# Optimization experiments

Hardware: AMD Instinct MI355X
Metric: run time of the kernel (lower is better)

The kernel has to match this reference:

```python
import jax, jax.numpy as jnp
import numpy as np

B, S, D, H, SE, DE, DFF = 4, 1024, 1024, 16, 77, 768, 4096


def _ln(x, g, b, eps=1e-5):
    mu = jnp.mean(x, axis=-1, keepdims=True)
    var = jnp.mean((x - mu) ** 2, axis=-1, keepdims=True)
    return (x - mu) * jax.lax.rsqrt(var + eps) * g + b


def _split_heads(x, heads):
    b, s, d = x.shape
    return x.reshape(b, s, heads, d // heads).transpose(0, 2, 1, 3)  # b h s hd


def _attn(q, k, v, heads):
    # memory_efficient_attention equivalent: softmax(q k^T * scale) v, per head
    q, k, v = _split_heads(q, heads), _split_heads(k, heads), _split_heads(v, heads)
    scale = q.shape[-1] ** -0.5
    scores = jnp.einsum('bhqd,bhkd->bhqk', q, k) * scale
    probs = jax.nn.softmax(scores, axis=-1)
    o = jnp.einsum('bhqk,bhkd->bhqd', probs, v)
    b, h, s, hd = o.shape
    return o.transpose(0, 2, 1, 3).reshape(b, s, h * hd)


def _geglu_ff(x, w1, b1, w2, b2):
    proj = x @ w1 + b1
    a, gate = jnp.split(proj, 2, axis=-1)
    return (a * jax.nn.gelu(gate)) @ w2 + b2


def _forward(h1, h2, enc, wq, wk, wv, wqc, wo, bo, ln1g, ln1b, ln2g, ln2b,
             w2q, w2k, w2v, w2o, b2o, wff1, bff1, wff2, bff2):
    # norm1
    n1 = _ln(h1, ln1g[0], ln1b[0])
    n2 = _ln(h2, ln1g[1], ln1b[1])
    # dual-stream uni-direction attention (self + cross with swapped K/V)
    q1, k1, v1, q1c = n1 @ wq[0], n1 @ wk[0], n1 @ wv[0], n1 @ wqc[0]
    q2, k2, v2, q2c = n2 @ wq[1], n2 @ wk[1], n2 @ wv[1], n2 @ wqc[1]
    a1 = _attn(q1, k1, v1, H) + _attn(q1c, k2, v2, H)
    a2 = _attn(q2, k2, v2, H) + _attn(q2c, k1, v1, H)
    a1 = a1 @ wo[0] + bo[0]
    a2 = a2 @ wo[1] + bo[1]
    h1 = h1 + a1
    h2 = h2 + a2
    # cross attention to encoder states (attn2)
    n1 = _ln(h1, ln2g[0], ln2b[0])
    n2 = _ln(h2, ln2g[1], ln2b[1])
    c1 = _attn(n1 @ w2q[0], enc @ w2k[0], enc @ w2v[0], H) @ w2o[0] + b2o[0]
    c2 = _attn(n2 @ w2q[1], enc @ w2k[1], enc @ w2v[1], H) @ w2o[1] + b2o[1]
    h1 = h1 + c1
    h2 = h2 + c2
    # feed-forward (GEGLU), applied to norm2 output exactly as in source
    h1 = h1 + _geglu_ff(n1, wff1[0], bff1[0], wff2[0], bff2[0])
    h2 = h2 + _geglu_ff(n2, wff1[1], bff1[1], wff2[1], bff2[1])
    return (h1, h2)


def setup_inputs() -> dict:
    key = jax.random.key(0)
    ks = jax.random.split(key, 16)
    f = lambda k, shp: jax.random.normal(k, shp, jnp.float32) * 0.02
    return {
        'h1': jax.random.normal(ks[0], (B, S, D), jnp.float32),
        'h2': jax.random.normal(ks[1], (B, S, D), jnp.float32),
        'enc': jax.random.normal(ks[2], (B, SE, DE), jnp.float32),
        'wq': f(ks[3], (2, D, D)), 'wk': f(ks[4], (2, D, D)),
        'wv': f(ks[5], (2, D, D)), 'wqc': f(ks[6], (2, D, D)),
        'wo': f(ks[7], (2, D, D)), 'bo': jnp.zeros((2, D), jnp.float32),
        'ln1g': jnp.ones((2, D), jnp.float32), 'ln1b': jnp.zeros((2, D), jnp.float32),
        'ln2g': jnp.ones((2, D), jnp.float32), 'ln2b': jnp.zeros((2, D), jnp.float32),
        'w2q': f(ks[8], (2, D, D)), 'w2k': f(ks[9], (2, DE, D)),
        'w2v': f(ks[10], (2, DE, D)), 'w2o': f(ks[11], (2, D, D)),
        'b2o': jnp.zeros((2, D), jnp.float32),
        'wff1': f(ks[12], (2, D, 2 * DFF)), 'bff1': jnp.zeros((2, 2 * DFF), jnp.float32),
        'wff2': f(ks[13], (2, DFF, D)), 'bff2': jnp.zeros((2, D), jnp.float32),
    }


def reference(h1, h2, enc, wq, wk, wv, wqc, wo, bo, ln1g, ln1b, ln2g, ln2b,
              w2q, w2k, w2v, w2o, b2o, wff1, bff1, wff2, bff2):
    return _forward(h1, h2, enc, wq, wk, wv, wqc, wo, bo, ln1g, ln1b, ln2g, ln2b,
                    w2q, w2k, w2v, w2o, b2o, wff1, bff1, wff2, bff2)
```

## Files before the change

kernel.cpp:

```cpp
#include <hip/hip_runtime.h>

typedef unsigned short u16;
typedef short v8s __attribute__((ext_vector_type(8)));
typedef float v4f __attribute__((ext_vector_type(4)));

__device__ __forceinline__ float bf2f(u16 u) {
  union { unsigned u; float f; } c; c.u = ((unsigned)u) << 16; return c.f;
}
__device__ __forceinline__ u16 f2bf(float x) {
  union { float f; unsigned u; } c; c.f = x;
  unsigned r = c.u + 0x7fffu + ((c.u >> 16) & 1u);
  return (u16)(r >> 16);
}
__device__ __forceinline__ v4f vzero() { v4f z; z[0]=0.f; z[1]=0.f; z[2]=0.f; z[3]=0.f; return z; }
__device__ __forceinline__ v4f mfma16(v8s a, v8s b, v4f c) {
  return __builtin_amdgcn_mfma_f32_16x16x32_bf16(a, b, c, 0, 0, 0);
}
__device__ __forceinline__ void async_lds16(const void* g, void* l) {
  __builtin_amdgcn_global_load_lds((__attribute__((address_space(1))) void*)g,
                                   (__attribute__((address_space(3))) void*)l, 16, 0, 0);
}
__device__ __forceinline__ float gelu_f(float x) {
  return 0.5f * x * (1.f + tanhf(0.7978845608028654f * (x + 0.044715f * x * x * x)));
}

__global__ void detect_k(const unsigned* __restrict__ p, unsigned* __restrict__ flag) {
  if (threadIdx.x == 0) {
    flag[0] = (p[0] == 0x3F803F80u) ? 1u : 0u;
    flag[1] = 0u;
  }
}

__global__ __launch_bounds__(256) void cvt_k(const unsigned* __restrict__ flag,
    const void* __restrict__ src, u16* __restrict__ dst, int n) {
  int i = (blockIdx.x * 256 + threadIdx.x) * 8;
  if (i >= n) return;
  if (*flag) {
    *(uint4*)(dst + i) = *(const uint4*)((const u16*)src + i);
  } else {
    const float* s = (const float*)src + i;
    #pragma unroll
    for (int j = 0; j < 8; ++j) dst[i + j] = f2bf(s[j]);
  }
}

__global__ __launch_bounds__(256) void tr_k(const unsigned* __restrict__ flag,
    const void* __restrict__ in, u16* __restrict__ out, int R, int C, long outZS) {
  __shared__ u16 tile[32][33];
  size_t zin = (size_t)blockIdx.z * R * C;
  size_t zout = (size_t)blockIdx.z * outZS;
  int c0 = blockIdx.x * 32, r0 = blockIdx.y * 32;
  int tx = threadIdx.x & 31, ty = threadIdx.x >> 5;
  unsigned isbf = *flag;
  const u16* inb = (const u16*)in + zin;
  const float* inf = (const float*)in + zin;
  #pragma unroll
  for (int i = ty; i < 32; i += 8) {
    size_t idx = (size_t)(r0 + i) * C + c0 + tx;
    tile[i][tx] = isbf ? inb[idx] : f2bf(inf[idx]);
  }
  __syncthreads();
  out += zout;
  #pragma unroll
  for (int i = ty; i < 32; i += 8) out[(size_t)(c0 + i) * R + r0 + tx] = tile[tx][i];
}

__global__ __launch_bounds__(256) void vtr_k(const u16* __restrict__ in, u16* __restrict__ out) {
  __shared__ u16 tile[32][33];
  int z = blockIdx.z >> 2, b = blockIdx.z & 3;
  const u16* ip = in + (size_t)z * 16777216 + (size_t)b * 4194304 + 2048;
  u16* op = out + (size_t)z * 4194304 + (size_t)b * 1048576;
  int k0 = blockIdx.x * 32, d0 = blockIdx.y * 32;
  int tx = threadIdx.x & 31, ty = threadIdx.x >> 5;
  #pragma unroll
  for (int i = ty; i < 32; i += 8)
    tile[i][tx] = ip[(size_t)(k0 + i) * 4096 + d0 + tx];
  __syncthreads();
  #pragma unroll
  for (int i = ty; i < 32; i += 8)
    op[(size_t)(d0 + i) * 1024 + k0 + tx] = tile[tx][i];
}

__global__ __launch_bounds__(256) void ln_k(const unsigned* __restrict__ flag,
    const void* __restrict__ src0, const void* __restrict__ src1,
    const u16* __restrict__ gw, const u16* __restrict__ bw, u16* __restrict__ out) {
  int z = blockIdx.y;
  const void* src = z ? src1 : src0;
  out += (size_t)z * 4194304; gw += z * 1024; bw += z * 1024;
  int row = blockIdx.x, t = threadIdx.x;
  unsigned isbf = *flag;
  float4 v;
  if (isbf) {
    uint2 d = ((const uint2*)((const u16*)src + (size_t)row * 1024))[t];
    v.x = bf2f((u16)(d.x & 0xffffu)); v.y = bf2f((u16)(d.x >> 16));
    v.z = bf2f((u16)(d.y & 0xffffu)); v.w = bf2f((u16)(d.y >> 16));
  } else {
    v = ((const float4*)((const float*)src + (size_t)row * 1024))[t];
  }
  float s = v.x + v.y + v.z + v.w;
  float s2 = v.x * v.x + v.y * v.y + v.z * v.z + v.w * v.w;
  #pragma unroll
  for (int o = 32; o; o >>= 1) { s += __shfl_down(s, o); s2 += __shfl_down(s2, o); }
  __shared__ float red[8];
  int w = t >> 6;
  if ((t & 63) == 0) { red[w] = s; red[4 + w] = s2; }
  __syncthreads();
  if (t == 0) {
    red[0] = red[0] + red[1] + red[2] + red[3];
    red[4] = red[4] + red[5] + red[6] + red[7];
  }
  __syncthreads();
  float mu = red[0] * (1.f / 1024.f);
  float var = red[4] * (1.f / 1024.f) - mu * mu;
  float rstd = rsqrtf(var + 1e-5f);
  int c = t * 4;
  float xs[4] = { v.x, v.y, v.z, v.w };
  #pragma unroll
  for (int j = 0; j < 4; ++j) {
    float g = bf2f(gw[c + j]), bb = bf2f(bw[c + j]);
    out[(size_t)row * 1024 + c + j] = f2bf((xs[j] - mu) * rstd * g + bb);
  }
}

template<int EPI>
__global__ __launch_bounds__(256, 2) void gemm_bt(
    const u16* __restrict__ A, const u16* __restrict__ Bt,
    int M, int N, int K, int lda, int ldb, int ldc,
    const u16* __restrict__ bias, const u16* aux,
    float* __restrict__ resF, void* __restrict__ outB,
    long zsA, long zsB, long zsC, int zsBias,
    const void* rin0, const void* rin1,
    const unsigned* __restrict__ flagp)
{
  int z = blockIdx.z;
  A += (size_t)z * zsA;
  Bt += (size_t)z * zsB;
  size_t zc = (size_t)z * zsC;
  unsigned isbf = 0;
  if (EPI == 4 || EPI == 5) isbf = *flagp;
  const void* rin = (EPI == 5) ? (z ? rin1 : rin0) : nullptr;
  __shared__ alignas(16) u16 As[128 * 64];
  __shared__ alignas(16) u16 Bs[128 * 64];
  int tid = threadIdx.x;
  int lane = tid & 63, wave = tid >> 6;
  int l15 = lane & 15, l4 = lane >> 4;
  int wm = wave & 1, wn = wave >> 1;
  int m0 = blockIdx.x * 128, n0 = blockIdx.y * 128;
  v4f acc[4][4];
  #pragma unroll
  for (int i = 0; i < 4; ++i)
    #pragma unroll
    for (int j = 0; j < 4; ++j) acc[i][j] = vzero();

  for (int k0 = 0; k0 < K; k0 += 64) {
    #pragma unroll
    for (int it = 0; it < 4; ++it) {
      int sidx = it * 256 + tid;
      int r = sidx >> 3, cs = (sidx & 7) * 8;
      int ra = m0 + r; if (ra > M - 1) ra = M - 1;
      async_lds16(A + (size_t)ra * lda + k0 + cs, As + (size_t)(it * 256 + wave * 64) * 8);
      async_lds16(Bt + (size_t)(n0 + r) * ldb + k0 + cs, Bs + (size_t)(it * 256 + wave * 64) * 8);
    }
    __syncthreads();
    #pragma unroll
    for (int ks = 0; ks < 2; ++ks) {
      v8s af[4], bfr[4];
      #pragma unroll
      for (int i = 0; i < 4; ++i) {
        af[i]  = *(const v8s*)(As + (wm * 64 + i * 16 + l15) * 64 + ks * 32 + l4 * 8);
        bfr[i] = *(const v8s*)(Bs + (wn * 64 + i * 16 + l15) * 64 + ks * 32 + l4 * 8);
      }
      #pragma unroll
      for (int i = 0; i < 4; ++i)
        #pragma unroll
        for (int j = 0; j < 4; ++j)
          acc[i][j] = mfma16(af[i], bfr[j], acc[i][j]);
    }
    __syncthreads();
  }
  #pragma unroll
  for (int mt = 0; mt < 4; ++mt) {
    #pragma unroll
    for (int r = 0; r < 4; ++r) {
      int gr = m0 + wm * 64 + mt * 16 + l4 * 4 + r;
      if (gr >= M) continue;
      size_t ri = (size_t)gr * ldc;
      size_t ro = zc + ri;
      #pragma unroll
      for (int nt = 0; nt < 4; ++nt) {
        int gc = n0 + wn * 64 + nt * 16 + l15;
        float v = acc[mt][nt][r];
        if (bias) v += bf2f(bias[(size_t)z * zsBias + gc]);
        if (EPI == 0) ((u16*)outB)[ro + gc] = f2bf(v);
        else if (EPI == 1) ((u16*)outB)[ro + gc] = f2bf(gelu_f(v));
        else if (EPI == 2) ((u16*)outB)[ro + gc] = f2bf(v * bf2f(aux[ro + gc]));
        else if (EPI == 3) resF[ro + gc] += v;
        else if (EPI == 5) {
          float h = isbf ? bf2f(((const u16*)rin)[ri + gc]) : ((const float*)rin)[ri + gc];
          resF[ro + gc] = h + v;
        } else {
          float o = resF[ro + gc] + v;
          if (isbf) ((u16*)outB)[ro + gc] = f2bf(o);
          else ((float*)outB)[ro + gc] = o;
        }
      }
    }
  }
}

__global__ __launch_bounds__(256, 2) void flash_self_k(
    const u16* __restrict__ qkv, const u16* __restrict__ Vt, u16* __restrict__ O)
{
  __shared__ alignas(16) u16 Ksh[128 * 64];
  __shared__ alignas(16) u16 Vsh[64 * 128];
  __shared__ alignas(16) u16 Psh[4][16 * 128];
  int tid = threadIdx.x, lane = tid & 63, wave = tid >> 6;
  int l15 = lane & 15, l4 = lane >> 4;
  int h = blockIdx.y;
  int strm = blockIdx.z >> 2, b = blockIdx.z & 3;
  const size_t ZS = 16777216;
  const size_t BS = 4194304;
  int q0 = blockIdx.x * 64 + wave * 16;
  u16* pw = Psh[wave];
  int swz = l15 & 7;
  v4f res[4];
  #pragma unroll
  for (int i = 0; i < 4; ++i) res[i] = vzero();

  for (int sg = 0; sg < 2; ++sg) {
    int qcol = sg ? 3072 : 0;
    int ksrc = sg ? (strm ^ 1) : strm;
    const u16* Qb = qkv + (size_t)strm * ZS + (size_t)b * BS + qcol + h * 64;
    const u16* Kb = qkv + (size_t)ksrc * ZS + (size_t)b * BS + 1024 + h * 64;
    const u16* Vb = Vt + (size_t)ksrc * BS + (size_t)b * 1048576 + h * 65536;
    v8s qf0 = *(const v8s*)(Qb + (size_t)(q0 + l15) * 4096 + l4 * 8);
    v8s qf1 = *(const v8s*)(Qb + (size_t)(q0 + l15) * 4096 + l4 * 8 + 32);
    v4f oacc[4];
    #pragma unroll
    for (int i = 0; i < 4; ++i) oacc[i] = vzero();
    float mrun[4], lrun[4];
    #pragma unroll
    for (int r = 0; r < 4; ++r) { mrun[r] = -1e30f; lrun[r] = 0.f; }

    for (int c0 = 0; c0 < 1024; c0 += 128) {
      #pragma unroll
      for (int it = 0; it < 4; ++it) {
        int sidx = it * 256 + tid;
        int r = sidx >> 3, c = sidx & 7;
        async_lds16(Kb + (size_t)(c0 + r) * 4096 + ((c ^ (r & 7)) * 8),
                    Ksh + (size_t)(it * 256 + wave * 64) * 8);
      }
      #pragma unroll
      for (int it = 0; it < 4; ++it) {
        int sidx = it * 256 + tid;
        int d = sidx >> 4, c = sidx & 15;
        async_lds16(Vb + (size_t)d * 1024 + c0 + ((c ^ (d & 15)) * 8),
                    Vsh + (size_t)(it * 256 + wave * 64) * 8);
      }
      __syncthreads();
      v4f s[4][2];
      #pragma unroll
      for (int g = 0; g < 4; ++g) { s[g][0] = vzero(); s[g][1] = vzero(); }
      __builtin_amdgcn_s_setprio(1);
      #pragma unroll
      for (int g = 0; g < 4; ++g) {
        int rb0 = (g * 32 + l15) * 64, rb1 = rb0 + 16 * 64;
        v8s k00 = *(const v8s*)(Ksh + rb0 + ((l4 ^ swz) * 8));
        v8s k10 = *(const v8s*)(Ksh + rb1 + ((l4 ^ swz) * 8));
        v8s k01 = *(const v8s*)(Ksh + rb0 + (((4 + l4) ^ swz) * 8));
        v8s k11 = *(const v8s*)(Ksh + rb1 + (((4 + l4) ^ swz) * 8));
        s[g][0] = mfma16(qf0, k00, s[g][0]);
        s[g][1] = mfma16(qf0, k10, s[g][1]);
        s[g][0] = mfma16(qf1, k01, s[g][0]);
        s[g][1] = mfma16(qf1, k11, s[g][1]);
      }
      __builtin_amdgcn_s_setprio(0);
      float alpha[4];
      #pragma unroll
      for (int r = 0; r < 4; ++r) {
        int row = l4 * 4 + r;
        float x[8];
        #pragma unroll
        for (int g = 0; g < 4; ++g) {
          x[2 * g]     = s[g][0][r] * 0.125f;
          x[2 * g + 1] = s[g][1][r] * 0.125f;
        }
        float tm = fmaxf(fmaxf(fmaxf(x[0], x[1]), fmaxf(x[2], x[3])),
                         fmaxf(fmaxf(x[4], x[5]), fmaxf(x[6], x[7])));
        #pragma unroll
        for (int o = 8; o; o >>= 1) tm = fmaxf(tm, __shfl_xor(tm, o));
        float mn = fmaxf(mrun[r], tm);
        alpha[r] = __expf(mrun[r] - mn);
        mrun[r] = mn;
        float rs = 0.f;
        #pragma unroll
        for (int j = 0; j < 8; ++j) {
          float p = __expf(x[j] - mn);
          rs += p;
          int col = (j >> 1) * 32 + (j & 1) * 16 + l15;
          pw[row * 128 + (((col >> 3) ^ row) * 8) + (col & 7)] = f2bf(p);
        }
        #pragma unroll
        for (int o = 8; o; o >>= 1) rs += __shfl_xor(rs, o);
        lrun[r] = lrun[r] * alpha[r] + rs;
      }
      #pragma unroll
      for (int nt = 0; nt < 4; ++nt)
        #pragma unroll
        for (int r = 0; r < 4; ++r) oacc[nt][r] *= alpha[r];
      __builtin_amdgcn_s_setprio(1);
      #pragma unroll
      for (int g = 0; g < 4; ++g) {
        v8s pa = *(const v8s*)(pw + l15 * 128 + (((g * 4 + l4) ^ l15) * 8));
        #pragma unroll
        for (int nt = 0; nt < 4; ++nt) {
          int vr = nt * 16 + l15;
          v8s vb = *(const v8s*)(Vsh + vr * 128 + (((g * 4 + l4) ^ (vr & 15)) * 8));
          oacc[nt] = mfma16(pa, vb, oacc[nt]);
        }
      }
      __builtin_amdgcn_s_setprio(0);
      __syncthreads();
    }
    #pragma unroll
    for (int r = 0; r < 4; ++r) {
      float inv = 1.f / lrun[r];
      #pragma unroll
      for (int nt = 0; nt < 4; ++nt) res[nt][r] += oacc[nt][r] * inv;
    }
  }
  #pragma unroll
  for (int nt = 0; nt < 4; ++nt) {
    #pragma unroll
    for (int r = 0; r < 4; ++r) {
      int gq = q0 + l4 * 4 + r;
      size_t oi = (size_t)strm * BS + ((size_t)b * 1024 + gq) * 1024 + h * 64 + nt * 16 + l15;
      O[oi] = f2bf(res[nt][r]);
    }
  }
}

__global__ __launch_bounds__(256, 2) void flash_cross_k(
    const u16* __restrict__ Q, const u16* __restrict__ KV, u16* __restrict__ O)
{
  __shared__ alignas(16) u16 Ksh[128 * 64];
  __shared__ alignas(16) unsigned VshT[64 * 68];
  __shared__ alignas(16) u16 Psh[4][16 * 128];
  int tid = threadIdx.x, lane = tid & 63, wave = tid >> 6;
  int l15 = lane & 15, l4 = lane >> 4;
  int h = blockIdx.y;
  int strm = blockIdx.z >> 2, b = blockIdx.z & 3;
  const u16* Qb = Q + (size_t)strm * 4194304 + (size_t)b * 1048576 + h * 64;
  const u16* Kb = KV + (size_t)strm * 630784 + (size_t)b * 157696 + h * 64;
  const u16* Vb = Kb + 1024;
  int q0 = blockIdx.x * 64 + wave * 16;
  u16* pw = Psh[wave];
  int swz = l15 & 7;
  v8s qf0 = *(const v8s*)(Qb + (size_t)(q0 + l15) * 1024 + l4 * 8);
  v8s qf1 = *(const v8s*)(Qb + (size_t)(q0 + l15) * 1024 + l4 * 8 + 32);

  #pragma unroll
  for (int it = 0; it < 4; ++it) {
    int sidx = it * 256 + tid;
    int r = sidx >> 3, c = sidx & 7;
    int gk = r > 76 ? 76 : r;
    async_lds16(Kb + (size_t)gk * 2048 + ((c ^ (r & 7)) * 8),
                Ksh + (size_t)(it * 256 + wave * 64) * 8);
  }
  #pragma unroll
  for (int it = 0; it < 2; ++it) {
    int tt = it * 256 + tid;
    int kp = tt & 63, dsg = tt >> 6;
    int gk0 = kp * 2, gk1 = kp * 2 + 1;
    if (gk0 > 76) gk0 = 76;
    if (gk1 > 76) gk1 = 76;
    v8s v0 = *(const v8s*)(Vb + (size_t)gk0 * 2048 + dsg * 8);
    v8s v1 = *(const v8s*)(Vb + (size_t)gk1 * 2048 + dsg * 8);
    #pragma unroll
    for (int j = 0; j < 8; ++j) {
      unsigned pk = (unsigned)(u16)v0[j] | ((unsigned)(u16)v1[j] << 16);
      VshT[(dsg * 8 + j) * 68 + kp] = pk;
    }
  }
  __syncthreads();
  v4f s[4][2];
  #pragma unroll
  for (int g = 0; g < 4; ++g) { s[g][0] = vzero(); s[g][1] = vzero(); }
  __builtin_amdgcn_s_setprio(1);
  #pragma unroll
  for (int g = 0; g < 4; ++g) {
    int rb0 = (g * 32 + l15) * 64, rb1 = rb0 + 16 * 64;
    v8s k00 = *(const v8s*)(Ksh + rb0 + ((l4 ^ swz) * 8));
    v8s k10 = *(const v8s*)(Ksh + rb1 + ((l4 ^ swz) * 8));
    v8s k01 = *(const v8s*)(Ksh + rb0 + (((4 + l4) ^ swz) * 8));
    v8s k11 = *(const v8s*)(Ksh + rb1 + (((4 + l4) ^ swz) * 8));
    s[g][0] = mfma16(qf0, k00, s[g][0]);
    s[g][1] = mfma16(qf0, k10, s[g][1]);
    s[g][0] = mfma16(qf1, k01, s[g][0]);
    s[g][1] = mfma16(qf1, k11, s[g][1]);
  }
  __builtin_amdgcn_s_setprio(0);
  float lsum[4];
  #pragma unroll
  for (int r = 0; r < 4; ++r) {
    int row = l4 * 4 + r;
    float x[8];
    #pragma unroll
    for (int g = 0; g < 4; ++g) {
      bool ok0 = (g * 32 + l15) < 77, ok1 = (g * 32 + 16 + l15) < 77;
      x[2 * g]     = ok0 ? s[g][0][r] * 0.125f : -1e30f;
      x[2 * g + 1] = ok1 ? s[g][1][r] * 0.125f : -1e30f;
    }
    float tm = fmaxf(fmaxf(fmaxf(x[0], x[1]), fmaxf(x[2], x[3])),
                     fmaxf(fmaxf(x[4], x[5]), fmaxf(x[6], x[7])));
    #pragma unroll
    for (int o = 8; o; o >>= 1) tm = fmaxf(tm, __shfl_xor(tm, o));
    float rs = 0.f;
    #pragma unroll
    for (int j = 0; j < 8; ++j) {
      float p = __expf(x[j] - tm);
      rs += p;
      int col = (j >> 1) * 32 + (j & 1) * 16 + l15;
      pw[row * 128 + (((col >> 3) ^ row) * 8) + (col & 7)] = f2bf(p);
    }
    #pragma unroll
    for (int o = 8; o; o >>= 1) rs += __shfl_xor(rs, o);
    lsum[r] = rs;
  }
  v4f oacc[4];
  #pragma unroll
  for (int i = 0; i < 4; ++i) oacc[i] = vzero();
  __builtin_amdgcn_s_setprio(1);
  #pragma unroll
  for (int g = 0; g < 4; ++g) {
    v8s pa = *(const v8s*)(pw + l15 * 128 + (((g * 4 + l4) ^ l15) * 8));
    #pragma unroll
    for (int nt = 0; nt < 4; ++nt) {
      v8s vb = *(const v8s*)((const u16*)VshT + (nt * 16 + l15) * 136 + g * 32 + l4 * 8);
      oacc[nt] = mfma16(pa, vb, oacc[nt]);
    }
  }
  __builtin_amdgcn_s_setprio(0);
  #pragma unroll
  for (int nt = 0; nt < 4; ++nt) {
    #pragma unroll
    for (int r = 0; r < 4; ++r) {
      int gq = q0 + l4 * 4 + r;
      size_t oi = (size_t)strm * 4194304 + ((size_t)b * 1024 + gq) * 1024 + h * 64 + nt * 16 + l15;
      O[oi] = f2bf(oacc[nt][r] / lsum[r]);
    }
  }
}

extern "C" void kernel_launch(void* const* d_in, const int* in_sizes, int n_in,
                              void* d_out, int out_size, void* d_ws, size_t ws_size,
                              hipStream_t stream)
{
  (void)in_sizes; (void)n_in; (void)out_size;
  const void* h1   = d_in[0];
  const void* h2   = d_in[1];
  const void* enc  = d_in[2];
  const void* wq   = d_in[3];
  const void* wk   = d_in[4];
  const void* wv   = d_in[5];
  const void* wqc  = d_in[6];
  const void* wo   = d_in[7];
  const void* bo   = d_in[8];
  const void* ln1g = d_in[9];
  const void* ln1b = d_in[10];
  const void* ln2g = d_in[11];
  const void* ln2b = d_in[12];
  const void* w2q  = d_in[13];
  const void* w2k  = d_in[14];
  const void* w2v  = d_in[15];
  const void* w2o  = d_in[16];
  const void* b2o  = d_in[17];
  const void* wff1 = d_in[18];
  const void* bff1 = d_in[19];
  const void* wff2 = d_in[20];
  const void* bff2 = d_in[21];

  const size_t S1 = 4194304;
  const size_t W1 = 1048576;
  const size_t QS = 16777216;
  const size_t NE = 236544;

  char* base = (char*)d_ws;
  size_t off = 0;
  auto AL = [&](size_t n) { size_t r = off; off += (n + 255) & ~(size_t)255; return r; };
  size_t o_flag   = AL(256);
  size_t o_pb     = AL(30720 * 2);
  size_t o_encB   = AL(NE * 2);
  size_t o_wqkvT  = AL(2 * 4 * W1 * 2);
  size_t o_woT    = AL(2 * W1 * 2);
  size_t o_w2qT   = AL(2 * W1 * 2);
  size_t o_w2oT   = AL(2 * W1 * 2);
  size_t o_w2kvT  = AL(2 * 2048 * 768 * 2);
  size_t o_wff1T  = AL(2 * 8192 * 1024 * 2);
  size_t o_wff2T  = AL(2 * 4096 * 1024 * 2);
  size_t o_hw     = AL(2 * S1 * 4);
  size_t o_n      = AL(2 * S1 * 2);
  size_t o_qkv    = AL(2 * QS * 2);
  size_t o_ab     = AL(2 * S1 * 2);
  if (ws_size < off) return;

  unsigned* flagp = (unsigned*)(base + o_flag);
  const unsigned* zerop = flagp + 1;
  u16* pb = (u16*)(base + o_pb);
  u16* boB   = pb + 0;
  u16* b2oB  = pb + 2048;
  u16* ln1gB = pb + 4096;
  u16* ln1bB = pb + 6144;
  u16* ln2gB = pb + 8192;
  u16* ln2bB = pb + 10240;
  u16* bff2B = pb + 12288;
  u16* bff1B = pb + 14336;
  u16* encB  = (u16*)(base + o_encB);
  u16* wqkvT = (u16*)(base + o_wqkvT);
  u16* woT   = (u16*)(base + o_woT);
  u16* w2qT  = (u16*)(base + o_w2qT);
  u16* w2oT  = (u16*)(base + o_w2oT);
  u16* w2kvT = (u16*)(base + o_w2kvT);
  u16* wff1T = (u16*)(base + o_wff1T);
  u16* wff2T = (u16*)(base + o_wff2T);
  float* hw  = (float*)(base + o_hw);
  u16* n1    = (u16*)(base + o_n);
  u16* qkv   = (u16*)(base + o_qkv);
  u16* a1b   = (u16*)(base + o_ab);
  u16* q1x   = qkv;
  u16* c1b   = qkv + 2 * S1;
  u16* kencv = qkv + 4 * S1;
  u16* gelu  = qkv;
  u16* vtb   = n1;

  auto tr = [&](const void* ip, u16* op, int R, int C, long outZS) {
    dim3 g(C / 32, R / 32, 2);
    tr_k<<<g, 256, 0, stream>>>(flagp, ip, op, R, C, outZS);
  };
  auto cvt = [&](const void* ip, u16* op, int n) {
    cvt_k<<<(n / 8 + 255) / 256, 256, 0, stream>>>(flagp, ip, op, n);
  };
  auto gemm = [&](int epi, const u16* Ap, const u16* Bp, int M, int N, int K,
                  int lda, int ldb, int ldc, const u16* bias, const u16* aux,
                  float* resF, void* oB, int nz, long zsA, long zsB, long zsC, int zsBias,
                  const void* rin0, const void* rin1) {
    dim3 g((M + 127) / 128, N / 128, nz);
    switch (epi) {
      case 0: gemm_bt<0><<<g, 256, 0, stream>>>(Ap, Bp, M, N, K, lda, ldb, ldc, bias, aux, resF, oB, zsA, zsB, zsC, zsBias, rin0, rin1, flagp); break;
      case 1: gemm_bt<1><<<g, 256, 0, stream>>>(Ap, Bp, M, N, K, lda, ldb, ldc, bias, aux, resF, oB, zsA, zsB, zsC, zsBias, rin0, rin1, flagp); break;
      case 2: gemm_bt<2><<<g, 256, 0, stream>>>(Ap, Bp, M, N, K, lda, ldb, ldc, bias, aux, resF, oB, zsA, zsB, zsC, zsBias, rin0, rin1, flagp); break;
      case 3: gemm_bt<3><<<g, 256, 0, stream>>>(Ap, Bp, M, N, K, lda, ldb, ldc, bias, aux, resF, oB, zsA, zsB, zsC, zsBias, rin0, rin1, flagp); break;
      case 4: gemm_bt<4><<<g, 256, 0, stream>>>(Ap, Bp, M, N, K, lda, ldb, ldc, bias, aux, resF, oB, zsA, zsB, zsC, zsBias, rin0, rin1, flagp); break;
      default: gemm_bt<5><<<g, 256, 0, stream>>>(Ap, Bp, M, N, K, lda, ldb, ldc, bias, aux, resF, oB, zsA, zsB, zsC, zsBias, rin0, rin1, flagp); break;
    }
  };

  detect_k<<<1, 64, 0, stream>>>((const unsigned*)ln1g, flagp);
  cvt(bo, boB, 2048);     cvt(b2o, b2oB, 2048);
  cvt(ln1g, ln1gB, 2048); cvt(ln1b, ln1bB, 2048);
  cvt(ln2g, ln2gB, 2048); cvt(ln2b, ln2bB, 2048);
  cvt(bff2, bff2B, 2048); cvt(bff1, bff1B, 16384);
  cvt(enc, encB, (int)NE);
  tr(wq,  wqkvT + 0 * W1, 1024, 1024, 4 * (long)W1);
  tr(wk,  wqkvT + 1 * W1, 1024, 1024, 4 * (long)W1);
  tr(wv,  wqkvT + 2 * W1, 1024, 1024, 4 * (long)W1);
  tr(wqc, wqkvT + 3 * W1, 1024, 1024, 4 * (long)W1);
  tr(wo,  woT,  1024, 1024, (long)W1);
  tr(w2q, w2qT, 1024, 1024, (long)W1);
  tr(w2o, w2oT, 1024, 1024, (long)W1);
  tr(w2k, w2kvT + 0,          768, 1024, 2048L * 768);
  tr(w2v, w2kvT + 1024 * 768, 768, 1024, 2048L * 768);
  tr(wff1, wff1T, 1024, 8192, 8192L * 1024);
  tr(wff2, wff2T, 4096, 1024, 4096L * 1024);
  ln_k<<<dim3(4096, 2), 256, 0, stream>>>(flagp, h1, h2, ln1gB, ln1bB, n1);
  gemm(0, n1, wqkvT, 4096, 4096, 1024, 1024, 1024, 4096, nullptr, nullptr, nullptr, qkv,
       2, (long)S1, 4 * (long)W1, (long)QS, 0, nullptr, nullptr);
  vtr_k<<<dim3(32, 32, 8), 256, 0, stream>>>(qkv, vtb);
  flash_self_k<<<dim3(16, 16, 8), 256, 0, stream>>>(qkv, vtb, a1b);
  gemm(5, a1b, woT, 4096, 1024, 1024, 1024, 1024, 1024, boB, nullptr, hw, nullptr,
       2, (long)S1, (long)W1, (long)S1, 1024, h1, h2);
  ln_k<<<dim3(4096, 2), 256, 0, stream>>>(zerop, hw, hw + S1, ln2gB, ln2bB, n1);
  gemm(0, n1, w2qT, 4096, 1024, 1024, 1024, 1024, 1024, nullptr, nullptr, nullptr, q1x,
       2, (long)S1, (long)W1, (long)S1, 0, nullptr, nullptr);
  gemm(0, encB, w2kvT, 308, 2048, 768, 768, 768, 2048, nullptr, nullptr, nullptr, kencv,
       2, 0, 2048L * 768, 308L * 2048, 0, nullptr, nullptr);
  flash_cross_k<<<dim3(16, 16, 8), 256, 0, stream>>>(q1x, kencv, c1b);
  gemm(3, c1b, w2oT, 4096, 1024, 1024, 1024, 1024, 1024, b2oB, nullptr, hw, nullptr,
       2, (long)S1, (long)W1, (long)S1, 1024, nullptr, nullptr);
  gemm(1, n1, wff1T + 4096 * 1024, 4096, 4096, 1024, 1024, 1024, 4096,
       bff1B + 4096, nullptr, nullptr, gelu, 2, (long)S1, 8192L * 1024, (long)QS, 8192,
       nullptr, nullptr);
  gemm(2, n1, wff1T, 4096, 4096, 1024, 1024, 1024, 4096,
       bff1B, gelu, nullptr, gelu, 2, (long)S1, 8192L * 1024, (long)QS, 8192,
       nullptr, nullptr);
  gemm(4, gelu, wff2T, 4096, 1024, 4096, 4096, 4096, 1024,
       bff2B, nullptr, hw, d_out, 2, (long)QS, 4096L * 1024, (long)S1, 1024,
       nullptr, nullptr);
}
```

Baseline: 1.222 ms.

## Add 256x256-tile 8-wave GEMM with 4-stage async pipeline for large projections

Introduces a new GEMM kernel with 256x256 output tiles, 512 threads, and a 4-slot LDS ring filled by async global-to-LDS loads using explicit vmcnt gating and priority hints. It is used for the QKV projection and the two GEGLU first-layer GEMMs, which are all N=4096, K=1024. The larger tile raises arithmetic intensity and cuts redundant operand loads. The cost is 128 KB of LDS per block, heavy accumulator register pressure, and only 512 blocks per launch, which may reduce occupancy or leave some tail imbalance.

```diff
diff --git a/kernel.cpp b/kernel.cpp
--- a/kernel.cpp
+++ b/kernel.cpp
@@ -203,6 +203,151 @@
           if (isbf) ((u16*)outB)[ro + gc] = f2bf(o);
           else ((float*)outB)[ro + gc] = o;
         }
+      }
+    }
+  }
+}
+
+template<int EPI>
+__global__ __launch_bounds__(512, 2) void gemm256(
+    const u16* __restrict__ A, const u16* __restrict__ Bt,
+    int M, int N, int K, int lda, int ldb, int ldc,
+    const u16* __restrict__ bias, const u16* aux, void* __restrict__ outB,
+    long zsA, long zsB, long zsC, int zsBias)
+{
+  __shared__ alignas(16) u16 As[4][8192];
+  __shared__ alignas(16) u16 Bs[4][8192];
+  int z = blockIdx.z;
+  A += (size_t)z * zsA;
+  Bt += (size_t)z * zsB;
+  size_t zc = (size_t)z * zsC;
+  int tid = threadIdx.x, lane = tid & 63, wave = tid >> 6;
+  int l15 = lane & 15, l4 = lane >> 4;
+  int wm = wave >> 2, wn = wave & 3;
+  int m0 = blockIdx.x * 256, n0 = blockIdx.y * 256;
+  int sa = l4 ^ ((l15 >> 1) & 3);
+  int nG = K >> 5;
+
+  v4f acc[8][4];
+  #pragma unroll
+  for (int i = 0; i < 8; ++i)
+    #pragma unroll
+    for (int j = 0; j < 4; ++j) acc[i][j] = vzero();
+
+  auto stageA = [&](int g) {
+    int sl = g & 3;
+    #pragma unroll
+    for (int l = 0; l < 2; ++l) {
+      int sidx = l * 512 + tid;
+      int r = sidx >> 2, c = sidx & 3;
+      async_lds16(A + (size_t)(m0 + r) * lda + g * 32 + ((c ^ ((sidx >> 3) & 3)) * 8),
+                  As[sl] + (size_t)(l * 512 + wave * 64) * 8);
+    }
+  };
+  auto stageB = [&](int g) {
+    int sl = g & 3;
+    #pragma unroll
+    for (int l = 0; l < 2; ++l) {
+      int sidx = l * 512 + tid;
+      int r = sidx >> 2, c = sidx & 3;
+      async_lds16(Bt + (size_t)(n0 + r) * ldb + g * 32 + ((c ^ ((sidx >> 3) & 3)) * 8),
+                  Bs[sl] + (size_t)(l * 512 + wave * 64) * 8);
+    }
+  };
+  auto gate = [&](int cnt) {
+    if (cnt >= 2)      asm volatile("s_waitcnt vmcnt(8)" ::: "memory");
+    else if (cnt == 1) asm volatile("s_waitcnt vmcnt(4)" ::: "memory");
+    else               asm volatile("s_waitcnt vmcnt(0)" ::: "memory");
+    __builtin_amdgcn_sched_barrier(0);
+  };
+
+  stageA(0); stageB(0);
+  if (1 < nG) { stageA(1); stageB(1); }
+  if (2 < nG) { stageA(2); stageB(2); }
+  gate((1 < nG) + (2 < nG));
+  __builtin_amdgcn_s_barrier();
+
+  auto kstep = [&](int t, int s0, int s1) {
+    int g0 = 2 * t, g1 = 2 * t + 1;
+    const u16* a0 = As[s0]; const u16* b0 = Bs[s0];
+    const u16* a1 = As[s1]; const u16* b1 = Bs[s1];
+    v8s af[4], bf[4];
+    #pragma unroll
+    for (int i = 0; i < 4; ++i) {
+      af[i] = *(const v8s*)(a0 + ((wm * 128 + i * 16 + l15) * 4 + sa) * 8);
+      bf[i] = *(const v8s*)(b0 + ((wn * 64 + i * 16 + l15) * 4 + sa) * 8);
+    }
+    if (g0 + 3 < nG) stageA(g0 + 3);
+    __builtin_amdgcn_s_barrier();
+    __builtin_amdgcn_s_setprio(1);
+    #pragma unroll
+    for (int i = 0; i < 4; ++i)
+      #pragma unroll
+      for (int j = 0; j < 4; ++j) acc[i][j] = mfma16(af[i], bf[j], acc[i][j]);
+    __builtin_amdgcn_s_setprio(0);
+    __builtin_amdgcn_s_barrier();
+    #pragma unroll
+    for (int i = 0; i < 4; ++i)
+      af[i] = *(const v8s*)(a0 + ((wm * 128 + 64 + i * 16 + l15) * 4 + sa) * 8);
+    if (g0 + 3 < nG) stageB(g0 + 3);
+    __builtin_amdgcn_s_barrier();
+    __builtin_amdgcn_s_setprio(1);
+    #pragma unroll
+    for (int i = 0; i < 4; ++i)
+      #pragma unroll
+      for (int j = 0; j < 4; ++j) acc[4 + i][j] = mfma16(af[i], bf[j], acc[4 + i][j]);
+    __builtin_amdgcn_s_setprio(0);
+    gate((g0 + 2 < nG) + (g0 + 3 < nG));
+    __builtin_amdgcn_s_barrier();
+    #pragma unroll
+    for (int i = 0; i < 4; ++i) {
+      af[i] = *(const v8s*)(a1 + ((wm * 128 + i * 16 + l15) * 4 + sa) * 8);
+      bf[i] = *(const v8s*)(b1 + ((wn * 64 + i * 16 + l15) * 4 + sa) * 8);
+    }
+    if (g1 + 3 < nG) stageA(g1 + 3);
+    __builtin_amdgcn_s_barrier();
+    __builtin_amdgcn_s_setprio(1);
+    #pragma unroll
+    for (int i = 0; i < 4; ++i)
+      #pragma unroll
+      for (int j = 0; j < 4; ++j) acc[i][j] = mfma16(af[i], bf[j], acc[i][j]);
+    __builtin_amdgcn_s_setprio(0);
+    __builtin_amdgcn_s_barrier();
+    #pragma unroll
+    for (int i = 0; i < 4; ++i)
+      af[i] = *(const v8s*)(a1 + ((wm * 128 + 64 + i * 16 + l15) * 4 + sa) * 8);
+    if (g1 + 3 < nG) stageB(g1 + 3);
+    __builtin_amdgcn_s_barrier();
+    __builtin_amdgcn_s_setprio(1);
+    #pragma unroll
+    for (int i = 0; i < 4; ++i)
+      #pragma unroll
+      for (int j = 0; j < 4; ++j) acc[4 + i][j] = mfma16(af[i], bf[j], acc[4 + i][j]);
+    __builtin_amdgcn_s_setprio(0);
+    gate((g1 + 2 < nG) + (g1 + 3 < nG));
+    __builtin_amdgcn_s_barrier();
+  };
+
+  int Ksteps = K >> 6;
+  for (int t = 0; t < Ksteps; t += 2) {
+    kstep(t, 0, 1);
+    kstep(t + 1, 2, 3);
+  }
+
+  #pragma unroll
+  for (int mi = 0; mi < 8; ++mi) {
+    #pragma unroll
+    for (int rr = 0; rr < 4; ++rr) {
+      int gr = m0 + wm * 128 + mi * 16 + l4 * 4 + rr;
+      size_t ro = zc + (size_t)gr * ldc;
+      #pragma unroll
+      for (int ni = 0; ni < 4; ++ni) {
+        int gc = n0 + wn * 64 + ni * 16 + l15;
+        float v = acc[mi][ni][rr];
+        if (bias) v += bf2f(bias[(size_t)z * zsBias + gc]);
+        if (EPI == 0) ((u16*)outB)[ro + gc] = f2bf(v);
+        else if (EPI == 1) ((u16*)outB)[ro + gc] = f2bf(gelu_f(v));
+        else ((u16*)outB)[ro + gc] = f2bf(v * bf2f(aux[ro + gc]));
       }
     }
   }
@@ -573,8 +718,8 @@
   tr(wff1, wff1T, 1024, 8192, 8192L * 1024);
   tr(wff2, wff2T, 4096, 1024, 4096L * 1024);
   ln_k<<<dim3(4096, 2), 256, 0, stream>>>(flagp, h1, h2, ln1gB, ln1bB, n1);
-  gemm(0, n1, wqkvT, 4096, 4096, 1024, 1024, 1024, 4096, nullptr, nullptr, nullptr, qkv,
-       2, (long)S1, 4 * (long)W1, (long)QS, 0, nullptr, nullptr);
+  gemm256<0><<<dim3(16, 16, 2), 512, 0, stream>>>(n1, wqkvT, 4096, 4096, 1024,
+      1024, 1024, 4096, nullptr, nullptr, qkv, (long)S1, 4 * (long)W1, (long)QS, 0);
   vtr_k<<<dim3(32, 32, 8), 256, 0, stream>>>(qkv, vtb);
   flash_self_k<<<dim3(16, 16, 8), 256, 0, stream>>>(qkv, vtb, a1b);
   gemm(5, a1b, woT, 4096, 1024, 1024, 1024, 1024, 1024, boB, nullptr, hw, nullptr,
@@ -587,12 +732,10 @@
   flash_cross_k<<<dim3(16, 16, 8), 256, 0, stream>>>(q1x, kencv, c1b);
   gemm(3, c1b, w2oT, 4096, 1024, 1024, 1024, 1024, 1024, b2oB, nullptr, hw, nullptr,
        2, (long)S1, (long)W1, (long)S1, 1024, nullptr, nullptr);
-  gemm(1, n1, wff1T + 4096 * 1024, 4096, 4096, 1024, 1024, 1024, 4096,
-       bff1B + 4096, nullptr, nullptr, gelu, 2, (long)S1, 8192L * 1024, (long)QS, 8192,
-       nullptr, nullptr);
-  gemm(2, n1, wff1T, 4096, 4096, 1024, 1024, 1024, 4096,
-       bff1B, gelu, nullptr, gelu, 2, (long)S1, 8192L * 1024, (long)QS, 8192,
-       nullptr, nullptr);
+  gemm256<1><<<dim3(16, 16, 2), 512, 0, stream>>>(n1, wff1T + 4096 * 1024, 4096, 4096, 1024,
+      1024, 1024, 4096, bff1B + 4096, nullptr, gelu, (long)S1, 8192L * 1024, (long)QS, 8192);
+  gemm256<2><<<dim3(16, 16, 2), 512, 0, stream>>>(n1, wff1T, 4096, 4096, 1024,
+      1024, 1024, 4096, bff1B, gelu, gelu, (long)S1, 8192L * 1024, (long)QS, 8192);
   gemm(4, gelu, wff2T, 4096, 1024, 4096, 4096, 4096, 1024,
        bff2B, nullptr, hw, d_out, 2, (long)QS, 4096L * 1024, (long)S1, 1024,
        nullptr, nullptr);
```

New measurement: 1.199 ms. Within noise of the previous version (-1.9%).
